# Kernel optimization log

Measured on AMD Instinct MI355X. Metric: run time of the kernel, lower is better.

The kernel has to match this reference:

```python
import jax, jax.numpy as jnp
import numpy as np

DEPTH = 4
HEADS = 8
DIM = 512
HIDDEN = int(DIM * 2.0)  # mlp_ratio=2.0
K_HOPS = 4
EPS = 1e-5


def _layer_norm(x, g, b):
    m = jnp.mean(x, axis=-1, keepdims=True)
    v = jnp.mean(jnp.square(x - m), axis=-1, keepdims=True)
    return (x - m) * jax.lax.rsqrt(v + EPS) * g + b


def setup_inputs() -> dict:
    key = jax.random.key(0)
    ks = jax.random.split(key, 20)
    B, N, C = 2048, 17, DIM
    inp = {
        "x": jax.random.normal(ks[0], (B, N, C), jnp.float32),
        "Hstack": jax.random.uniform(ks[1], (K_HOPS, N, N), jnp.float32),
        "hop_logits_attn": jax.random.normal(ks[2], (HEADS, K_HOPS), jnp.float32),
        "rel_alpha": jax.random.normal(ks[3], (HEADS,), jnp.float32),
        # per-layer params stacked over depth
        "qkv_w": jax.random.normal(ks[4], (DEPTH, 3 * C, C), jnp.float32) * 0.02,
        "qkv_b": jnp.zeros((DEPTH, 3 * C), jnp.float32),
        "proj_w": jax.random.normal(ks[5], (DEPTH, C, C), jnp.float32) * 0.02,
        "proj_b": jnp.zeros((DEPTH, C), jnp.float32),
        "ln1_g": jnp.ones((DEPTH, C), jnp.float32),
        "ln1_b": jnp.zeros((DEPTH, C), jnp.float32),
        "ln2_g": jnp.ones((DEPTH, C), jnp.float32),
        "ln2_b": jnp.zeros((DEPTH, C), jnp.float32),
        "fc1_w": jax.random.normal(ks[6], (DEPTH, HIDDEN, C), jnp.float32) * 0.02,
        "fc1_b": jnp.zeros((DEPTH, HIDDEN), jnp.float32),
        "fc2_w": jax.random.normal(ks[7], (DEPTH, C, HIDDEN), jnp.float32) * 0.02,
        "fc2_b": jnp.zeros((DEPTH, C), jnp.float32),
    }
    return inp


def _block(x, Hstack, hop_logits_attn, rel_alpha, qkv_w, qkv_b, proj_w, proj_b,
           ln1_g, ln1_b, ln2_g, ln2_b, fc1_w, fc1_b, fc2_w, fc2_b):
    B, N, C = x.shape
    hd = C // HEADS
    scale = hd ** (-0.5)
    h = _layer_norm(x, ln1_g, ln1_b)
    qkv = h @ qkv_w.T + qkv_b  # [B,N,3C]
    qkv = qkv.reshape(B, N, 3, HEADS, hd).transpose(2, 0, 3, 1, 4)
    q, k, v = qkv[0], qkv[1], qkv[2]  # [B,H,N,hd]
    logits = jnp.einsum('bhnd,bhmd->bhnm', q, k) * scale
    # hop-based additive bias: softmax over hops, mixed into per-head bias
    w = jax.nn.softmax(hop_logits_attn, axis=-1)  # [H,K]
    B_head = jnp.einsum('hk,kij->hij', w, Hstack)  # [H,N,N]
    bias = rel_alpha[:, None, None] * B_head
    logits = logits + bias[None]
    attn = jax.nn.softmax(logits, axis=-1)
    out = jnp.einsum('bhnm,bhmd->bhnd', attn, v)
    out = out.transpose(0, 2, 1, 3).reshape(B, N, C)
    out = out @ proj_w.T + proj_b
    x = x + out
    h2 = _layer_norm(x, ln2_g, ln2_b)
    h2 = jax.nn.gelu(h2 @ fc1_w.T + fc1_b, approximate=False)
    x = x + (h2 @ fc2_w.T + fc2_b)
    return x


def reference(x, Hstack, hop_logits_attn, rel_alpha, qkv_w, qkv_b, proj_w, proj_b,
              ln1_g, ln1_b, ln2_g, ln2_b, fc1_w, fc1_b, fc2_w, fc2_b):
    for d in range(DEPTH):
        x = _block(x, Hstack, hop_logits_attn, rel_alpha,
                   qkv_w[d], qkv_b[d], proj_w[d], proj_b[d],
                   ln1_g[d], ln1_b[d], ln2_g[d], ln2_b[d],
                   fc1_w[d], fc1_b[d], fc2_w[d], fc2_b[d])
    return x
```

## Files before the change

kernel.cpp:

```cpp
#include <hip/hip_runtime.h>

#define DEPTHL 4
#define NHEADS 8
#define DIMC 512
#define HIDDENC 1024
#define NTOK 17
#define NROWS (2048*NTOK)

typedef __attribute__((ext_vector_type(8))) short s8v;
typedef __attribute__((ext_vector_type(4))) float f4v;
typedef __attribute__((ext_vector_type(4))) short s4v;

static __device__ __forceinline__ float bf2f(short s) {
  unsigned u = ((unsigned)(unsigned short)s) << 16;
  return __builtin_bit_cast(float, u);
}
static __device__ __forceinline__ short f2bf(float f) {
  unsigned u = __builtin_bit_cast(unsigned, f);
  u += 0x7fffu + ((u >> 16) & 1u);
  return (short)(u >> 16);
}

static __device__ __forceinline__ void load_lds16(const void* g, void* l) {
  __builtin_amdgcn_global_load_lds(
      (const __attribute__((address_space(1))) unsigned int*)g,
      (__attribute__((address_space(3))) unsigned int*)l, 16, 0, 0);
}

__global__ __launch_bounds__(256) void f2bf_kernel(const float* __restrict__ in,
                                                   short* __restrict__ out, int n4) {
  int i = blockIdx.x * 256 + threadIdx.x;
  if (i < n4) {
    float4 v = ((const float4*)in)[i];
    s4v o;
    o[0] = f2bf(v.x); o[1] = f2bf(v.y); o[2] = f2bf(v.z); o[3] = f2bf(v.w);
    ((s4v*)out)[i] = o;
  }
}

__global__ __launch_bounds__(256) void ln_kernel(const float* __restrict__ x,
    const float* __restrict__ g, const float* __restrict__ b,
    short* __restrict__ h) {
  int row = blockIdx.x * 4 + (threadIdx.x >> 6);
  int lane = threadIdx.x & 63;
  const float* xr = x + (size_t)row * DIMC + lane * 8;
  float4 v0 = *(const float4*)xr;
  float4 v1 = *(const float4*)(xr + 4);
  float s = v0.x + v0.y + v0.z + v0.w + v1.x + v1.y + v1.z + v1.w;
  #pragma unroll
  for (int o = 32; o > 0; o >>= 1) s += __shfl_xor(s, o, 64);
  float mean = s * (1.0f / 512.0f);
  float d0 = v0.x-mean, d1 = v0.y-mean, d2 = v0.z-mean, d3 = v0.w-mean;
  float d4 = v1.x-mean, d5 = v1.y-mean, d6 = v1.z-mean, d7 = v1.w-mean;
  float vs = d0*d0+d1*d1+d2*d2+d3*d3+d4*d4+d5*d5+d6*d6+d7*d7;
  #pragma unroll
  for (int o = 32; o > 0; o >>= 1) vs += __shfl_xor(vs, o, 64);
  float rstd = rsqrtf(vs * (1.0f / 512.0f) + 1e-5f);
  const float* gp = g + lane * 8;
  const float* bp = b + lane * 8;
  float4 g0 = *(const float4*)gp, g1 = *(const float4*)(gp + 4);
  float4 b0 = *(const float4*)bp, b1 = *(const float4*)(bp + 4);
  s8v o;
  o[0] = f2bf(d0 * rstd * g0.x + b0.x);
  o[1] = f2bf(d1 * rstd * g0.y + b0.y);
  o[2] = f2bf(d2 * rstd * g0.z + b0.z);
  o[3] = f2bf(d3 * rstd * g0.w + b0.w);
  o[4] = f2bf(d4 * rstd * g1.x + b1.x);
  o[5] = f2bf(d5 * rstd * g1.y + b1.y);
  o[6] = f2bf(d6 * rstd * g1.z + b1.z);
  o[7] = f2bf(d7 * rstd * g1.w + b1.w);
  *(s8v*)(h + (size_t)row * DIMC + lane * 8) = o;
}

enum { EPI_BF16 = 0, EPI_RES_F32 = 1, EPI_GELU_BF16 = 2 };

template<int K, int EPI>
__global__ __launch_bounds__(256) void gemm_bt(
    const short* __restrict__ A, const short* __restrict__ Bm,
    const float* __restrict__ bias, const float* __restrict__ res,
    void* __restrict__ outp, int N) {
  __shared__ __align__(16) short As[128 * 64];
  __shared__ __align__(16) short Bs[128 * 64];
  const int tid = threadIdx.x;
  const int wave = tid >> 6, lane = tid & 63;
  const int m0 = blockIdx.y * 128, n0 = blockIdx.x * 128;
  const int wr = wave >> 1, wc = wave & 1;
  f4v acc[4][4] = {};

  for (int k0 = 0; k0 < K; k0 += 64) {
    #pragma unroll
    for (int j = 0; j < 4; ++j) {
      int base_slot = j * 256 + wave * 64;
      int slot = base_slot + lane;
      int row = slot >> 3;
      int kc = (slot & 7) * 8;
      const short* gA = A + (size_t)(m0 + row) * K + k0 + kc;
      load_lds16(gA, &As[base_slot * 8]);
      const short* gB = Bm + (size_t)(n0 + row) * K + k0 + kc;
      load_lds16(gB, &Bs[base_slot * 8]);
    }
    __syncthreads();
    #pragma unroll
    for (int kk = 0; kk < 2; ++kk) {
      s8v af[4], bfr[4];
      int kof = kk * 32 + (lane >> 4) * 8;
      #pragma unroll
      for (int i = 0; i < 4; ++i) {
        af[i]  = *(const s8v*)&As[(wr * 64 + i * 16 + (lane & 15)) * 64 + kof];
        bfr[i] = *(const s8v*)&Bs[(wc * 64 + i * 16 + (lane & 15)) * 64 + kof];
      }
      #pragma unroll
      for (int i = 0; i < 4; ++i)
        #pragma unroll
        for (int j2 = 0; j2 < 4; ++j2)
          acc[i][j2] = __builtin_amdgcn_mfma_f32_16x16x32_bf16(af[i], bfr[j2], acc[i][j2], 0, 0, 0);
    }
    __syncthreads();
  }

  const int cb = n0 + wc * 64 + (lane & 15);
  const int rb = m0 + wr * 64 + ((lane >> 4) << 2);
  #pragma unroll
  for (int i = 0; i < 4; ++i) {
    #pragma unroll
    for (int j2 = 0; j2 < 4; ++j2) {
      int n = cb + j2 * 16;
      float bs = bias[n];
      #pragma unroll
      for (int r = 0; r < 4; ++r) {
        int m = rb + i * 16 + r;
        float v = acc[i][j2][r] + bs;
        size_t off = (size_t)m * N + n;
        if constexpr (EPI == EPI_RES_F32) {
          ((float*)outp)[off] = res[off] + v;
        } else if constexpr (EPI == EPI_GELU_BF16) {
          float gv = 0.5f * v * (1.0f + erff(v * 0.70710678118654752f));
          ((short*)outp)[off] = f2bf(gv);
        } else {
          ((short*)outp)[off] = f2bf(v);
        }
      }
    }
  }
}

__global__ __launch_bounds__(256) void attnbias_kernel(const float* __restrict__ H,
    const float* __restrict__ hop_logits, const float* __restrict__ rel_alpha,
    float* __restrict__ battn) {
  int t = threadIdx.x;
  for (int e = t; e < NHEADS * NTOK * NTOK; e += 256) {
    int h = e / (NTOK * NTOK);
    int nm = e - h * NTOK * NTOK;
    float l0 = hop_logits[h * 4 + 0], l1 = hop_logits[h * 4 + 1];
    float l2 = hop_logits[h * 4 + 2], l3 = hop_logits[h * 4 + 3];
    float mx = fmaxf(fmaxf(l0, l1), fmaxf(l2, l3));
    float e0 = expf(l0 - mx), e1 = expf(l1 - mx), e2 = expf(l2 - mx), e3 = expf(l3 - mx);
    float inv = 1.0f / (e0 + e1 + e2 + e3);
    float bsum = (e0 * H[0 * 289 + nm] + e1 * H[1 * 289 + nm] +
                  e2 * H[2 * 289 + nm] + e3 * H[3 * 289 + nm]) * inv;
    battn[e] = rel_alpha[h] * bsum;
  }
}

__global__ __launch_bounds__(256) void attn_kernel(const short* __restrict__ qkv,
    const float* __restrict__ battn, short* __restrict__ out) {
  __shared__ __align__(16) short sq[4][NTOK * 64];
  __shared__ __align__(16) short sk[4][NTOK * 64];
  __shared__ __align__(16) short sv[4][NTOK * 64];
  __shared__ float sp[4][NTOK * 18];
  int w = threadIdx.x >> 6, lane = threadIdx.x & 63;
  int wid = blockIdx.x * 4 + w;
  int b = wid >> 3, h = wid & 7;

  for (int s = lane; s < NTOK * 8; s += 64) {
    int n = s >> 3, c8 = (s & 7) * 8;
    const short* rowp = qkv + (size_t)(b * NTOK + n) * 1536 + h * 64 + c8;
    *(s8v*)&sq[w][s * 8] = *(const s8v*)&rowp[0];
    *(s8v*)&sk[w][s * 8] = *(const s8v*)&rowp[512];
    *(s8v*)&sv[w][s * 8] = *(const s8v*)&rowp[1024];
  }
  __syncthreads();

  #pragma unroll
  for (int idx = 0; idx < 5; ++idx) {
    int e = idx * 64 + lane;
    int ec = e < 289 ? e : 288;
    int n = ec / 17, m = ec - n * 17;
    float acc = 0.f;
    #pragma unroll
    for (int c = 0; c < 8; ++c) {
      s8v qv = *(const s8v*)&sq[w][n * 64 + c * 8];
      s8v kv = *(const s8v*)&sk[w][m * 64 + c * 8];
      #pragma unroll
      for (int t = 0; t < 8; ++t) acc += bf2f(qv[t]) * bf2f(kv[t]);
    }
    if (e < 289) sp[w][n * 18 + m] = acc * 0.125f + battn[h * 289 + e];
  }
  __syncthreads();

  if (lane < NTOK) {
    float mx = -1e30f;
    #pragma unroll
    for (int m = 0; m < NTOK; ++m) mx = fmaxf(mx, sp[w][lane * 18 + m]);
    float pv[NTOK];
    float ssum = 0.f;
    #pragma unroll
    for (int m = 0; m < NTOK; ++m) { float ev = expf(sp[w][lane * 18 + m] - mx); pv[m] = ev; ssum += ev; }
    float inv = 1.0f / ssum;
    #pragma unroll
    for (int m = 0; m < NTOK; ++m) sp[w][lane * 18 + m] = pv[m] * inv;
  }
  __syncthreads();

  #pragma unroll
  for (int n = 0; n < NTOK; ++n) {
    float ov = 0.f;
    #pragma unroll
    for (int m = 0; m < NTOK; ++m) ov += sp[w][n * 18 + m] * bf2f(sv[w][m * 64 + lane]);
    out[(size_t)(b * NTOK + n) * DIMC + h * 64 + lane] = f2bf(ov);
  }
}

extern "C" void kernel_launch(void* const* d_in, const int* in_sizes, int n_in,
                              void* d_out, int out_size, void* d_ws, size_t ws_size,
                              hipStream_t stream) {
  const float* x_in       = (const float*)d_in[0];
  const float* Hstack     = (const float*)d_in[1];
  const float* hop_logits = (const float*)d_in[2];
  const float* rel_alpha  = (const float*)d_in[3];
  const float* qkv_w  = (const float*)d_in[4];
  const float* qkv_b  = (const float*)d_in[5];
  const float* proj_w = (const float*)d_in[6];
  const float* proj_b = (const float*)d_in[7];
  const float* ln1_g  = (const float*)d_in[8];
  const float* ln1_b  = (const float*)d_in[9];
  const float* ln2_g  = (const float*)d_in[10];
  const float* ln2_b  = (const float*)d_in[11];
  const float* fc1_w  = (const float*)d_in[12];
  const float* fc1_b  = (const float*)d_in[13];
  const float* fc2_w  = (const float*)d_in[14];
  const float* fc2_b  = (const float*)d_in[15];
  float* xout = (float*)d_out;

  short* wqkv  = (short*)d_ws;
  short* wproj = wqkv  + (size_t)4 * 1536 * 512;
  short* wfc1  = wproj + (size_t)4 * 512 * 512;
  short* wfc2  = wfc1  + (size_t)4 * 1024 * 512;
  float* battn = (float*)(wfc2 + (size_t)4 * 512 * 1024);
  short* hbuf   = (short*)(battn + 2432);
  short* qkvbuf = hbuf + (size_t)NROWS * 512;

  {
    int n4;
    n4 = 4 * 1536 * 512 / 4;
    f2bf_kernel<<<dim3((n4 + 255) / 256), dim3(256), 0, stream>>>(qkv_w, wqkv, n4);
    n4 = 4 * 512 * 512 / 4;
    f2bf_kernel<<<dim3((n4 + 255) / 256), dim3(256), 0, stream>>>(proj_w, wproj, n4);
    n4 = 4 * 1024 * 512 / 4;
    f2bf_kernel<<<dim3((n4 + 255) / 256), dim3(256), 0, stream>>>(fc1_w, wfc1, n4);
    n4 = 4 * 512 * 1024 / 4;
    f2bf_kernel<<<dim3((n4 + 255) / 256), dim3(256), 0, stream>>>(fc2_w, wfc2, n4);
  }
  attnbias_kernel<<<dim3(1), dim3(256), 0, stream>>>(Hstack, hop_logits, rel_alpha, battn);

  const int LNBLK = NROWS / 4;
  const dim3 B256(256);

  for (int d = 0; d < DEPTHL; ++d) {
    const float* xres = (d == 0) ? x_in : xout;
    ln_kernel<<<dim3(LNBLK), B256, 0, stream>>>(xres, ln1_g + d * 512, ln1_b + d * 512, hbuf);
    gemm_bt<512, EPI_BF16><<<dim3(1536 / 128, NROWS / 128), B256, 0, stream>>>(
        hbuf, wqkv + (size_t)d * 1536 * 512, qkv_b + d * 1536, nullptr, qkvbuf, 1536);
    attn_kernel<<<dim3(2048 * NHEADS / 4), B256, 0, stream>>>(qkvbuf, battn, hbuf);
    gemm_bt<512, EPI_RES_F32><<<dim3(512 / 128, NROWS / 128), B256, 0, stream>>>(
        hbuf, wproj + (size_t)d * 512 * 512, proj_b + d * 512, xres, xout, 512);
    ln_kernel<<<dim3(LNBLK), B256, 0, stream>>>(xout, ln2_g + d * 512, ln2_b + d * 512, hbuf);
    gemm_bt<512, EPI_GELU_BF16><<<dim3(1024 / 128, NROWS / 128), B256, 0, stream>>>(
        hbuf, wfc1 + (size_t)d * 1024 * 512, fc1_b + d * 1024, nullptr, qkvbuf, 1024);
    gemm_bt<1024, EPI_RES_F32><<<dim3(512 / 128, NROWS / 128), B256, 0, stream>>>(
        qkvbuf, wfc2 + (size_t)d * 512 * 1024, fc2_b + d * 512, xout, xout, 512);
  }
}
```

Baseline: 1.954 ms.

## Double-buffer GEMM LDS tiles with XOR swizzle and block-index remapping

Rewrites the bf16 GEMM so it stages the next K-tile into a second LDS buffer while MFMAs run on the current one, which removes the load-then-compute stall and one barrier per iteration. LDS column chunks are XOR-swizzled by row to avoid bank conflicts on the fragment reads. A 1D grid with a modulo-8 block remap is also introduced, presumably to spread neighbouring tiles across XCDs or improve L2 locality. LDS use doubles to 64KB per block, which can reduce occupancy.

```diff
diff --git a/kernel.cpp b/kernel.cpp
--- a/kernel.cpp
+++ b/kernel.cpp
@@ -26,6 +26,9 @@
       (const __attribute__((address_space(1))) unsigned int*)g,
       (__attribute__((address_space(3))) unsigned int*)l, 16, 0, 0);
 }
+
+#define BARX() asm volatile("s_barrier" ::: "memory")
+#define VMC0() asm volatile("s_waitcnt vmcnt(0)" ::: "memory")
 
 __global__ __launch_bounds__(256) void f2bf_kernel(const float* __restrict__ in,
                                                    short* __restrict__ out, int n4) {
@@ -75,62 +78,78 @@
 enum { EPI_BF16 = 0, EPI_RES_F32 = 1, EPI_GELU_BF16 = 2 };
 
 template<int K, int EPI>
-__global__ __launch_bounds__(256) void gemm_bt(
+__global__ __launch_bounds__(256) void gemm2p(
     const short* __restrict__ A, const short* __restrict__ Bm,
     const float* __restrict__ bias, const float* __restrict__ res,
-    void* __restrict__ outp, int N) {
-  __shared__ __align__(16) short As[128 * 64];
-  __shared__ __align__(16) short Bs[128 * 64];
+    void* __restrict__ outp, int N, int nbx) {
+  constexpr int NT = K / 64;
+  __shared__ __align__(16) short SA[2][8192];
+  __shared__ __align__(16) short SB[2][8192];
   const int tid = threadIdx.x;
   const int wave = tid >> 6, lane = tid & 63;
-  const int m0 = blockIdx.y * 128, n0 = blockIdx.x * 128;
+  const int l15 = lane & 15, l4 = lane >> 4;
+  const int nwg = gridDim.x, bid = blockIdx.x;
+  const int swz = (bid & 7) * (nwg >> 3) + (bid >> 3);
+  const int bx = swz % nbx, by = swz / nbx;
+  const int m0 = by * 128, n0 = bx * 128;
   const int wr = wave >> 1, wc = wave & 1;
+
   f4v acc[4][4] = {};
 
-  for (int k0 = 0; k0 < K; k0 += 64) {
-    #pragma unroll
-    for (int j = 0; j < 4; ++j) {
-      int base_slot = j * 256 + wave * 64;
-      int slot = base_slot + lane;
-      int row = slot >> 3;
-      int kc = (slot & 7) * 8;
-      const short* gA = A + (size_t)(m0 + row) * K + k0 + kc;
-      load_lds16(gA, &As[base_slot * 8]);
-      const short* gB = Bm + (size_t)(n0 + row) * K + k0 + kc;
-      load_lds16(gB, &Bs[base_slot * 8]);
-    }
-    __syncthreads();
+  auto stageT = [&](const short* __restrict__ mat, int row0, int k0, short* ldsb) {
+    #pragma unroll
+    for (int q = 0; q < 4; ++q) {
+      const int r = q * 32 + (tid >> 3), c = tid & 7;
+      const short* src = mat + (size_t)(row0 + r) * K + k0 + ((c ^ (r & 7)) << 3);
+      load_lds16(src, ldsb + q * 2048 + ((tid & ~63) << 3));
+    }
+  };
+
+  stageT(A, m0, 0, SA[0]);
+  stageT(Bm, n0, 0, SB[0]);
+  VMC0();
+  BARX();
+
+  #pragma unroll
+  for (int t = 0; t < NT; ++t) {
+    const int cur = t & 1;
+    if (t + 1 < NT) {
+      stageT(A, m0, (t + 1) * 64, SA[cur ^ 1]);
+      stageT(Bm, n0, (t + 1) * 64, SB[cur ^ 1]);
+    }
     #pragma unroll
     for (int kk = 0; kk < 2; ++kk) {
       s8v af[4], bfr[4];
-      int kof = kk * 32 + (lane >> 4) * 8;
       #pragma unroll
       for (int i = 0; i < 4; ++i) {
-        af[i]  = *(const s8v*)&As[(wr * 64 + i * 16 + (lane & 15)) * 64 + kof];
-        bfr[i] = *(const s8v*)&Bs[(wc * 64 + i * 16 + (lane & 15)) * 64 + kof];
+        const int Ra = wr * 64 + i * 16 + l15;
+        af[i] = *(const s8v*)&SA[cur][(Ra << 6) + (((kk * 4 + l4) ^ (Ra & 7)) << 3)];
+        const int Rb = wc * 64 + i * 16 + l15;
+        bfr[i] = *(const s8v*)&SB[cur][(Rb << 6) + (((kk * 4 + l4) ^ (Rb & 7)) << 3)];
       }
       #pragma unroll
       for (int i = 0; i < 4; ++i)
         #pragma unroll
-        for (int j2 = 0; j2 < 4; ++j2)
-          acc[i][j2] = __builtin_amdgcn_mfma_f32_16x16x32_bf16(af[i], bfr[j2], acc[i][j2], 0, 0, 0);
-    }
-    __syncthreads();
-  }
-
-  const int cb = n0 + wc * 64 + (lane & 15);
-  const int rb = m0 + wr * 64 + ((lane >> 4) << 2);
+        for (int j = 0; j < 4; ++j)
+          acc[i][j] = __builtin_amdgcn_mfma_f32_16x16x32_bf16(af[i], bfr[j], acc[i][j], 0, 0, 0);
+    }
+    if (t + 1 < NT) VMC0();
+    BARX();
+  }
+
+  const int cb = n0 + wc * 64 + l15;
+  const int rb = m0 + wr * 64 + (l4 << 2);
   #pragma unroll
   for (int i = 0; i < 4; ++i) {
     #pragma unroll
     for (int j2 = 0; j2 < 4; ++j2) {
-      int n = cb + j2 * 16;
-      float bs = bias[n];
+      const int n = cb + j2 * 16;
+      const float bs = bias[n];
       #pragma unroll
       for (int r = 0; r < 4; ++r) {
-        int m = rb + i * 16 + r;
-        float v = acc[i][j2][r] + bs;
-        size_t off = (size_t)m * N + n;
+        const int m = rb + i * 16 + r;
+        const float v = acc[i][j2][r] + bs;
+        const size_t off = (size_t)m * N + n;
         if constexpr (EPI == EPI_RES_F32) {
           ((float*)outp)[off] = res[off] + v;
         } else if constexpr (EPI == EPI_GELU_BF16) {
@@ -265,19 +284,20 @@
 
   const int LNBLK = NROWS / 4;
   const dim3 B256(256);
+  const int MB = NROWS / 128;
 
   for (int d = 0; d < DEPTHL; ++d) {
     const float* xres = (d == 0) ? x_in : xout;
     ln_kernel<<<dim3(LNBLK), B256, 0, stream>>>(xres, ln1_g + d * 512, ln1_b + d * 512, hbuf);
-    gemm_bt<512, EPI_BF16><<<dim3(1536 / 128, NROWS / 128), B256, 0, stream>>>(
-        hbuf, wqkv + (size_t)d * 1536 * 512, qkv_b + d * 1536, nullptr, qkvbuf, 1536);
+    gemm2p<512, EPI_BF16><<<dim3((1536 / 128) * MB), B256, 0, stream>>>(
+        hbuf, wqkv + (size_t)d * 1536 * 512, qkv_b + d * 1536, nullptr, qkvbuf, 1536, 1536 / 128);
     attn_kernel<<<dim3(2048 * NHEADS / 4), B256, 0, stream>>>(qkvbuf, battn, hbuf);
-    gemm_bt<512, EPI_RES_F32><<<dim3(512 / 128, NROWS / 128), B256, 0, stream>>>(
-        hbuf, wproj + (size_t)d * 512 * 512, proj_b + d * 512, xres, xout, 512);
+    gemm2p<512, EPI_RES_F32><<<dim3((512 / 128) * MB), B256, 0, stream>>>(
+        hbuf, wproj + (size_t)d * 512 * 512, proj_b + d * 512, xres, xout, 512, 512 / 128);
     ln_kernel<<<dim3(LNBLK), B256, 0, stream>>>(xout, ln2_g + d * 512, ln2_b + d * 512, hbuf);
-    gemm_bt<512, EPI_GELU_BF16><<<dim3(1024 / 128, NROWS / 128), B256, 0, stream>>>(
-        hbuf, wfc1 + (size_t)d * 1024 * 512, fc1_b + d * 1024, nullptr, qkvbuf, 1024);
-    gemm_bt<1024, EPI_RES_F32><<<dim3(512 / 128, NROWS / 128), B256, 0, stream>>>(
-        qkvbuf, wfc2 + (size_t)d * 512 * 1024, fc2_b + d * 512, xout, xout, 512);
-  }
-}
+    gemm2p<512, EPI_GELU_BF16><<<dim3((1024 / 128) * MB), B256, 0, stream>>>(
+        hbuf, wfc1 + (size_t)d * 1024 * 512, fc1_b + d * 1024, nullptr, qkvbuf, 1024, 1024 / 128);
+    gemm2p<1024, EPI_RES_F32><<<dim3((512 / 128) * MB), B256, 0, stream>>>(
+        qkvbuf, wfc2 + (size_t)d * 512 * 1024, fc2_b + d * 512, xout, xout, 512, 512 / 128);
+  }
+}
```

Result: faster. 1.831 ms (-6.3%).
